# Kernel tuning notes

Measured on AMD Instinct MI355X. Metric: run time of the kernel, lower is better.

## Reference

```python
import jax, jax.numpy as jnp
import numpy as np

BLOCK = 128  # fp8 block-quant block size (128, 128)


def dequant_block_fp8_weight(w, scale_inv):
    """w: [O, I] fp8-valued weights (stored as f32); scale_inv: [O//128, I//128].
    Dequant = per-(128,128)-block multiply by scale."""
    O, I = w.shape
    wb = w.reshape(O // BLOCK, BLOCK, I // BLOCK, BLOCK)
    wb = wb * scale_inv[:, None, :, None]
    return wb.reshape(O, I)


def setup_inputs() -> dict:
    key = jax.random.key(0)
    ks = jax.random.split(key, 7)
    H, F, T = 5120, 1536, 8192  # hidden, moe_intermediate, tokens
    x = jax.random.normal(ks[0], (T, H), dtype=jnp.float32)
    w_gate = jax.random.normal(ks[1], (F, H), dtype=jnp.float32)
    s_gate = jax.random.uniform(ks[2], (F // BLOCK, H // BLOCK), dtype=jnp.float32) * 0.01 + 1e-4
    w_up = jax.random.normal(ks[3], (F, H), dtype=jnp.float32)
    s_up = jax.random.uniform(ks[4], (F // BLOCK, H // BLOCK), dtype=jnp.float32) * 0.01 + 1e-4
    w_down = jax.random.normal(ks[5], (H, F), dtype=jnp.float32)
    s_down = jax.random.uniform(ks[6], (H // BLOCK, F // BLOCK), dtype=jnp.float32) * 0.01 + 1e-4
    return {"x": x, "w_gate": w_gate, "s_gate": s_gate, "w_up": w_up,
            "s_up": s_up, "w_down": w_down, "s_down": s_down}


def reference(x, w_gate, s_gate, w_up, s_up, w_down, s_down):
    # down_proj(silu(gate_proj(x)) * up_proj(x)), each Linear dequantizing
    # block-scaled fp8 weights first (bias=False everywhere).
    wg = dequant_block_fp8_weight(w_gate, s_gate).astype(x.dtype)
    wu = dequant_block_fp8_weight(w_up, s_up).astype(x.dtype)
    wd = dequant_block_fp8_weight(w_down, s_down).astype(x.dtype)
    gate = jnp.einsum('th,fh->tf', x, wg)  # [T, F]
    up = jnp.einsum('th,fh->tf', x, wu)    # [T, F]
    h = jax.nn.silu(gate) * up
    out = jnp.einsum('tf,hf->th', h, wd)   # [T, H]
    return out
```

## Files before the change

### kernel.cpp

```cpp
#include <hip/hip_runtime.h>


typedef __bf16 bf16x8 __attribute__((ext_vector_type(8)));
typedef float  f32x4  __attribute__((ext_vector_type(4)));

__device__ __forceinline__ void glds16(const __bf16* g, __bf16* l) {
  __builtin_amdgcn_global_load_lds(
      (const __attribute__((address_space(1))) void*)g,
      (__attribute__((address_space(3))) void*)l, 16, 0, 0);
}

__device__ __forceinline__ void chunk_rk(int c, int& row, int& k) {
  int s = c >> 6;
  int w = (c & 63) << 4;
  int wl = w ^ (((w >> 9) & 1) << 5) ^ (((w >> 7) & 1) << 4);
  row = (s << 4) + (wl >> 6);
  k = (wl & 63) >> 1;
}

#define BAR()                               \
  do {                                      \
    __builtin_amdgcn_sched_barrier(0);      \
    asm volatile("s_barrier" ::: "memory"); \
    __builtin_amdgcn_sched_barrier(0);      \
  } while (0)

#define LGKM0()                                        \
  do {                                                 \
    asm volatile("s_waitcnt lgkmcnt(0)" ::: "memory"); \
    __builtin_amdgcn_sched_barrier(0);                 \
  } while (0)

#define VMBAR(n)                                                       \
  do {                                                                 \
    __builtin_amdgcn_sched_barrier(0);                                 \
    asm volatile("s_waitcnt vmcnt(" #n ")\n\ts_barrier" ::: "memory"); \
    __builtin_amdgcn_sched_barrier(0);                                 \
  } while (0)

__device__ __forceinline__ void cast8(const float* __restrict__ in,
                                      __bf16* __restrict__ out, size_t idx) {
  f32x4 a = *(const f32x4*)(in + idx);
  f32x4 b = *(const f32x4*)(in + idx + 4);
  bf16x8 o;
#pragma unroll
  for (int i = 0; i < 4; ++i) { o[i] = (__bf16)a[i]; o[i + 4] = (__bf16)b[i]; }
  *(bf16x8*)(out + idx) = o;
}

__device__ __forceinline__ void dq_ilv(const float* __restrict__ w,
                                       const float* __restrict__ s,
                                       __bf16* __restrict__ wq, int r, int tid,
                                       int which) {
  unsigned idx = ((unsigned)r * 256u + (unsigned)tid) * 8u;
  unsigned f = idx / 5120u;
  unsigned h = idx - f * 5120u;
  float sc = s[(f >> 7) * 40 + (h >> 7)];
  f32x4 a = *(const f32x4*)(w + idx);
  f32x4 b = *(const f32x4*)(w + idx + 4);
  bf16x8 o;
#pragma unroll
  for (int i = 0; i < 4; ++i) {
    o[i] = (__bf16)(a[i] * sc);
    o[i + 4] = (__bf16)(b[i] * sc);
  }
  *(bf16x8*)(wq + (size_t)(2 * f + which) * 5120 + h) = o;
}

__device__ __forceinline__ void dq_wd(const float* __restrict__ w,
                                      const float* __restrict__ s,
                                      __bf16* __restrict__ o8, int r, int tid) {
  unsigned idx = ((unsigned)r * 256u + (unsigned)tid) * 8u;
  unsigned f = idx / 1536u;
  unsigned h = idx - f * 1536u;
  float sc = s[(f >> 7) * 12 + (h >> 7)];
  f32x4 a = *(const f32x4*)(w + idx);
  f32x4 b = *(const f32x4*)(w + idx + 4);
  bf16x8 o;
#pragma unroll
  for (int i = 0; i < 4; ++i) {
    o[i] = (__bf16)(a[i] * sc);
    o[i + 4] = (__bf16)(b[i] * sc);
  }
  *(bf16x8*)(o8 + idx) = o;
}

__global__ void prep(const float* __restrict__ x, const float* __restrict__ wg,
                     const float* __restrict__ sg, const float* __restrict__ wu,
                     const float* __restrict__ su, const float* __restrict__ wd,
                     const float* __restrict__ sd, __bf16* __restrict__ xb,
                     __bf16* __restrict__ wq, __bf16* __restrict__ wdq) {
  int bid = blockIdx.x;
  int tid = threadIdx.x;
  if (bid < 20480) {
    cast8(x, xb, ((size_t)bid * 256 + tid) * 8);
  } else if (bid < 24320) {
    dq_ilv(wg, sg, wq, bid - 20480, tid, 0);
  } else if (bid < 28160) {
    dq_ilv(wu, su, wq, bid - 24320, tid, 1);
  } else {
    dq_wd(wd, sd, wdq, bid - 28160, tid);
  }
}

template <bool FUSE_SILU, typename OutT>
__global__ __launch_bounds__(256, 2) void gemm_p(
    const __bf16* __restrict__ A, const __bf16* __restrict__ B,
    OutT* __restrict__ C, int M, int N, int K, int ldc, int nbx) {
  __shared__ __bf16 lds[3 * 12288];
  const int tid = threadIdx.x;
  const int lane = tid & 63;
  const int wave = tid >> 6;
  const int lr = lane & 15;

  const int nwg = gridDim.x;
  const int lb = (blockIdx.x & 7) * (nwg >> 3) + (blockIdx.x >> 3);
  const int bx = lb % nbx;
  const int by = lb / nbx;
  const int m0 = by * 128, n0 = bx * 256;

  int laneoff = (lr << 6) | ((lane >> 4) << 4);
  laneoff ^= ((lr & 2) << 3) | ((lr & 8) << 2);
  const int b_sub = wave << 2;

  int rr[4], kk[4];
  chunk_rk(tid, rr[0], kk[0]);
  chunk_rk(tid + 256, rr[1], kk[1]);
  chunk_rk(tid + 512, rr[2], kk[2]);
  chunk_rk(tid + 768, rr[3], kk[3]);
  const unsigned o0 = (unsigned)rr[0] * K + (unsigned)kk[0];
  const unsigned o1 = (unsigned)rr[1] * K + (unsigned)kk[1];
  const unsigned o2 = (unsigned)rr[2] * K + (unsigned)kk[2];
  const unsigned o3 = (unsigned)rr[3] * K + (unsigned)kk[3];
  const int d0 = tid << 3, d1 = (tid + 256) << 3;
  const int d2 = (tid + 512) << 3, d3 = (tid + 768) << 3;
  const __bf16* Ab = A + (size_t)m0 * K;
  const __bf16* Bb = B + (size_t)n0 * K;

  f32x4 acc[8][4] = {};
  bf16x8 af[4], bg[4];

  auto STAGE_P0 = [&](int t, int s) {
    __bf16* sb = lds + s * 12288;
    const unsigned ko = (unsigned)t << 5;
    glds16(Ab + (o0 + ko), sb + d0);
    glds16(Ab + (o1 + ko), sb + d1);
    glds16(Bb + (o0 + ko), sb + 4096 + d0);
    glds16(Bb + (o1 + ko), sb + 4096 + d1);
  };
  auto STAGE_P1 = [&](int t, int s) {
    __bf16* sb = lds + s * 12288;
    const unsigned ko = (unsigned)t << 5;
    glds16(Bb + (o2 + ko), sb + 4096 + d2);
    glds16(Bb + (o3 + ko), sb + 4096 + d3);
  };
  auto RD_AF = [&](const char* base, int h) {
#pragma unroll
    for (int i = 0; i < 4; ++i)
      af[i] = *(const bf16x8*)(base + (((h << 2) + i) << 10) + laneoff);
  };
  auto RD_BG = [&](const char* base) {
#pragma unroll
    for (int j = 0; j < 4; ++j)
      bg[j] = *(const bf16x8*)(base + 8192 + ((b_sub + j) << 10) + laneoff);
  };
  auto MFMA16 = [&](int h) {
    __builtin_amdgcn_s_setprio(1);
#pragma unroll
    for (int j = 0; j < 4; ++j)
#pragma unroll
      for (int i = 0; i < 4; ++i)
        acc[(h << 2) + i][j] = __builtin_amdgcn_mfma_f32_16x16x32_bf16(
            af[i], bg[j], acc[(h << 2) + i][j], 0, 0, 0);
    __builtin_amdgcn_s_setprio(0);
  };

  const int NT = K >> 5;

  STAGE_P0(0, 0);
  STAGE_P1(0, 0);
  STAGE_P0(1, 1);
  STAGE_P1(1, 1);
  VMBAR(6);

  int cur = 0, stg = 2;
  for (int t = 0; t < NT - 2; ++t) {
    const char* cb = (const char*)lds + cur * 24576;
    RD_AF(cb, 0);
    RD_BG(cb);
    STAGE_P0(t + 2, stg);
    BAR();
    LGKM0();
    MFMA16(0);
    BAR();
    RD_AF(cb, 1);
    STAGE_P1(t + 2, stg);
    BAR();
    LGKM0();
    MFMA16(1);
    VMBAR(6);
    cur = (cur == 2) ? 0 : cur + 1;
    stg = (stg == 2) ? 0 : stg + 1;
  }
  {
    const char* cb = (const char*)lds + cur * 24576;
    RD_AF(cb, 0);
    RD_BG(cb);
    BAR();
    LGKM0();
    MFMA16(0);
    BAR();
    RD_AF(cb, 1);
    BAR();
    LGKM0();
    MFMA16(1);
    VMBAR(0);
    cur = (cur == 2) ? 0 : cur + 1;
  }
  {
    const char* cb = (const char*)lds + cur * 24576;
    RD_AF(cb, 0);
    RD_BG(cb);
    LGKM0();
    MFMA16(0);
    RD_AF(cb, 1);
    LGKM0();
    MFMA16(1);
  }

  const int colb = n0 + (wave << 6) + lr;
  const int rowb = m0 + ((lane >> 4) << 2);
#pragma unroll
  for (int i = 0; i < 8; ++i)
#pragma unroll
    for (int j = 0; j < 4; ++j)
#pragma unroll
      for (int r = 0; r < 4; ++r) {
        if constexpr (FUSE_SILU) {
          float v = acc[i][j][r];
          float p = __shfl_xor(v, 1, 64);
          float g = (lane & 1) ? p : v;
          float u = (lane & 1) ? v : p;
          float hv = (g / (1.0f + __expf(-g))) * u;
          if ((lane & 1) == 0)
            C[(size_t)(rowb + i * 16 + r) * ldc + ((colb + j * 16) >> 1)] =
                (OutT)hv;
        } else {
          C[(size_t)(rowb + i * 16 + r) * ldc + (colb + j * 16)] =
              (OutT)acc[i][j][r];
        }
      }
}

extern "C" void kernel_launch(void* const* d_in, const int* in_sizes, int n_in,
                              void* d_out, int out_size, void* d_ws,
                              size_t ws_size, hipStream_t stream) {
  const int Hd = 5120, Fd = 1536, Td = 8192;
  const float* x = (const float*)d_in[0];
  const float* wg = (const float*)d_in[1];
  const float* sg = (const float*)d_in[2];
  const float* wu = (const float*)d_in[3];
  const float* su = (const float*)d_in[4];
  const float* wd = (const float*)d_in[5];
  const float* sd = (const float*)d_in[6];
  float* out = (float*)d_out;

  __bf16* ws = (__bf16*)d_ws;
  const size_t xsz = (size_t)Td * Hd;
  __bf16* xb = ws;
  __bf16* wq = xb + xsz;
  __bf16* wdq = wq + (size_t)2 * Fd * Hd;
  __bf16* hbuf = wdq + (size_t)Hd * Fd;

  prep<<<32000, 256, 0, stream>>>(x, wg, sg, wu, su, wd, sd, xb, wq, wdq);

  gemm_p<true, __bf16><<<768, 256, 0, stream>>>(xb, wq, hbuf, Td, 2 * Fd, Hd,
                                                Fd, 12);

  gemm_p<false, float><<<1280, 256, 0, stream>>>(hbuf, wdq, out, Td, Hd, Fd,
                                                 Hd, 20);
}
```

Measured before the change: 732.1 us.

## Switch GEMM inner loop from 16x16x32 to 32x32x16 bf16 MFMA tiles

Replaces the 16x16x32 MFMA tiling with 32x32x16 MFMAs: each wave now holds 4x2 32x32 accumulator tiles and reads 4 A and 2 B fragments per half-step instead of 4+4. The LDS swizzle in chunk_rk and the per-lane read offsets are changed to match the new fragment layout, and the epilogue row/column mapping follows the 32x32 output layout. The aim is fewer LDS fragment reads and fewer MFMA issues per unit of work. It risks new LDS bank conflicts and a less coalesced store pattern in the epilogue.

```diff
diff --git a/kernel.cpp b/kernel.cpp
--- a/kernel.cpp
+++ b/kernel.cpp
@@ -3,6 +3,7 @@
 
 typedef __bf16 bf16x8 __attribute__((ext_vector_type(8)));
 typedef float  f32x4  __attribute__((ext_vector_type(4)));
+typedef float  f32x16 __attribute__((ext_vector_type(16)));
 
 __device__ __forceinline__ void glds16(const __bf16* g, __bf16* l) {
   __builtin_amdgcn_global_load_lds(
@@ -13,7 +14,7 @@
 __device__ __forceinline__ void chunk_rk(int c, int& row, int& k) {
   int s = c >> 6;
   int w = (c & 63) << 4;
-  int wl = w ^ (((w >> 9) & 1) << 5) ^ (((w >> 7) & 1) << 4);
+  int wl = w ^ (((w >> 7) & 1) << 4) ^ (((w >> 8) & 1) << 5);
   row = (s << 4) + (wl >> 6);
   k = (wl & 63) >> 1;
 }
@@ -111,7 +112,6 @@
   const int tid = threadIdx.x;
   const int lane = tid & 63;
   const int wave = tid >> 6;
-  const int lr = lane & 15;
 
   const int nwg = gridDim.x;
   const int lb = (blockIdx.x & 7) * (nwg >> 3) + (blockIdx.x >> 3);
@@ -119,9 +119,10 @@
   const int by = lb / nbx;
   const int m0 = by * 128, n0 = bx * 256;
 
-  int laneoff = (lr << 6) | ((lane >> 4) << 4);
-  laneoff ^= ((lr & 2) << 3) | ((lr & 8) << 2);
-  const int b_sub = wave << 2;
+  const int hio = (((lane & 31) >> 4) << 10) | ((lane & 15) << 6);
+  const int swz = ((lane & 2) << 3) | ((lane & 4) << 3);
+  const int ko0 = (((lane >> 5) << 4) | 0) ^ swz;
+  const int ko1 = (((lane >> 5) << 4) | 32) ^ swz;
 
   int rr[4], kk[4];
   chunk_rk(tid, rr[0], kk[0]);
@@ -137,8 +138,8 @@
   const __bf16* Ab = A + (size_t)m0 * K;
   const __bf16* Bb = B + (size_t)n0 * K;
 
-  f32x4 acc[8][4] = {};
-  bf16x8 af[4], bg[4];
+  f32x16 acc[4][2] = {};
+  bf16x8 af[4], bg[2];
 
   auto STAGE_P0 = [&](int t, int s) {
     __bf16* sb = lds + s * 12288;
@@ -154,24 +155,22 @@
     glds16(Bb + (o2 + ko), sb + 4096 + d2);
     glds16(Bb + (o3 + ko), sb + 4096 + d3);
   };
-  auto RD_AF = [&](const char* base, int h) {
+  auto RD = [&](const char* cb, int ko) {
 #pragma unroll
     for (int i = 0; i < 4; ++i)
-      af[i] = *(const bf16x8*)(base + (((h << 2) + i) << 10) + laneoff);
-  };
-  auto RD_BG = [&](const char* base) {
-#pragma unroll
-    for (int j = 0; j < 4; ++j)
-      bg[j] = *(const bf16x8*)(base + 8192 + ((b_sub + j) << 10) + laneoff);
-  };
-  auto MFMA16 = [&](int h) {
+      af[i] = *(const bf16x8*)(cb + i * 2048 + hio + ko);
+#pragma unroll
+    for (int j = 0; j < 2; ++j)
+      bg[j] = *(const bf16x8*)(cb + 8192 + (wave << 12) + j * 2048 + hio + ko);
+  };
+  auto MFMA8 = [&] {
     __builtin_amdgcn_s_setprio(1);
 #pragma unroll
-    for (int j = 0; j < 4; ++j)
+    for (int j = 0; j < 2; ++j)
 #pragma unroll
       for (int i = 0; i < 4; ++i)
-        acc[(h << 2) + i][j] = __builtin_amdgcn_mfma_f32_16x16x32_bf16(
-            af[i], bg[j], acc[(h << 2) + i][j], 0, 0, 0);
+        acc[i][j] = __builtin_amdgcn_mfma_f32_32x32x16_bf16(af[i], bg[j],
+                                                            acc[i][j], 0, 0, 0);
     __builtin_amdgcn_s_setprio(0);
   };
 
@@ -186,56 +185,55 @@
   int cur = 0, stg = 2;
   for (int t = 0; t < NT - 2; ++t) {
     const char* cb = (const char*)lds + cur * 24576;
-    RD_AF(cb, 0);
-    RD_BG(cb);
+    RD(cb, ko0);
     STAGE_P0(t + 2, stg);
     BAR();
     LGKM0();
-    MFMA16(0);
-    BAR();
-    RD_AF(cb, 1);
+    MFMA8();
+    BAR();
+    RD(cb, ko1);
     STAGE_P1(t + 2, stg);
     BAR();
     LGKM0();
-    MFMA16(1);
+    MFMA8();
     VMBAR(6);
     cur = (cur == 2) ? 0 : cur + 1;
     stg = (stg == 2) ? 0 : stg + 1;
   }
   {
     const char* cb = (const char*)lds + cur * 24576;
-    RD_AF(cb, 0);
-    RD_BG(cb);
-    BAR();
-    LGKM0();
-    MFMA16(0);
-    BAR();
-    RD_AF(cb, 1);
-    BAR();
-    LGKM0();
-    MFMA16(1);
+    RD(cb, ko0);
+    BAR();
+    LGKM0();
+    MFMA8();
+    BAR();
+    RD(cb, ko1);
+    BAR();
+    LGKM0();
+    MFMA8();
     VMBAR(0);
     cur = (cur == 2) ? 0 : cur + 1;
   }
   {
     const char* cb = (const char*)lds + cur * 24576;
-    RD_AF(cb, 0);
-    RD_BG(cb);
-    LGKM0();
-    MFMA16(0);
-    RD_AF(cb, 1);
-    LGKM0();
-    MFMA16(1);
-  }
-
-  const int colb = n0 + (wave << 6) + lr;
-  const int rowb = m0 + ((lane >> 4) << 2);
-#pragma unroll
-  for (int i = 0; i < 8; ++i)
-#pragma unroll
-    for (int j = 0; j < 4; ++j)
-#pragma unroll
-      for (int r = 0; r < 4; ++r) {
+    RD(cb, ko0);
+    LGKM0();
+    MFMA8();
+    RD(cb, ko1);
+    LGKM0();
+    MFMA8();
+  }
+
+  const int colx = n0 + (wave << 6) + (lane & 31);
+  const int rbase = m0 + ((lane >> 5) << 2);
+#pragma unroll
+  for (int i = 0; i < 4; ++i)
+#pragma unroll
+    for (int j = 0; j < 2; ++j)
+#pragma unroll
+      for (int r = 0; r < 16; ++r) {
+        const int row = rbase + i * 32 + (r & 3) + ((r >> 2) << 3);
+        const int col = colx + j * 32;
         if constexpr (FUSE_SILU) {
           float v = acc[i][j][r];
           float p = __shfl_xor(v, 1, 64);
@@ -243,11 +241,9 @@
           float u = (lane & 1) ? v : p;
           float hv = (g / (1.0f + __expf(-g))) * u;
           if ((lane & 1) == 0)
-            C[(size_t)(rowb + i * 16 + r) * ldc + ((colb + j * 16) >> 1)] =
-                (OutT)hv;
+            C[(size_t)row * ldc + (col >> 1)] = (OutT)hv;
         } else {
-          C[(size_t)(rowb + i * 16 + r) * ldc + (colb + j * 16)] =
-              (OutT)acc[i][j][r];
+          C[(size_t)row * ldc + col] = (OutT)acc[i][j][r];
         }
       }
 }
```

After: 755.2 us. 3.2% more time.
